# Kernel optimization log

Measured on AMD Instinct MI355X. Metric: run time of the kernel, lower is better.

Reference implementation:

```python
import jax, jax.numpy as jnp
import numpy as np

B, S, D_MODEL, D_HEAD = 4, 4096, 512, 64


def setup_inputs() -> dict:
    key = jax.random.key(0)
    ks = jax.random.split(key, 9)
    s = 1.0 / np.sqrt(D_MODEL)
    return {
        "q_in": jax.random.normal(ks[0], (B, S, D_MODEL), jnp.float32),
        "k_in": jax.random.normal(ks[1], (B, S, D_MODEL), jnp.float32),
        "v_in": jax.random.normal(ks[2], (B, S, D_MODEL), jnp.float32),
        "Wq": jax.random.normal(ks[3], (D_HEAD, D_MODEL), jnp.float32) * s,
        "bq": jax.random.normal(ks[4], (D_HEAD,), jnp.float32) * s,
        "Wk": jax.random.normal(ks[5], (D_HEAD, D_MODEL), jnp.float32) * s,
        "bk": jax.random.normal(ks[6], (D_HEAD,), jnp.float32) * s,
        "Wv": jax.random.normal(ks[7], (D_HEAD, D_MODEL), jnp.float32) * s,
        "bv": jax.random.normal(ks[8], (D_HEAD,), jnp.float32) * s,
    }


def reference(q_in, k_in, v_in, Wq, bq, Wk, bk, Wv, bv):
    # Linear projections (torch nn.Linear: x @ W.T + b)
    q = jnp.einsum("bsd,hd->bsh", q_in, Wq) + bq  # [B,S,Dh]
    k = jnp.einsum("bsd,hd->bsh", k_in, Wk) + bk
    v = jnp.einsum("bsd,hd->bsh", v_in, Wv) + bv
    # Causal mask: -inf strictly above diagonal (generate_attention_mask, triu(1))
    sk = k.shape[1]
    mask = jnp.triu(jnp.full((q.shape[1], sk), -jnp.inf, dtype=q.dtype), k=1)
    scores = jnp.einsum("bqh,bkh->bqk", q, k) / jnp.sqrt(jnp.asarray(q.shape[-1], q.dtype))
    attn = jax.nn.softmax(scores + mask, axis=-1)  # [B,S,S]
    return jnp.einsum("bqk,bkh->bqh", attn, v)
```

## Files before the change

kernel.cpp:

```cpp
#include <hip/hip_runtime.h>
#include <hip/hip_bf16.h>

#define B_ 4
#define S_ 4096
#define DM 512
#define DH 64

#define NEG_BIG (-3.0e38f)
#define MCLAMP  (-1.0e30f)

typedef __attribute__((ext_vector_type(8))) short short8b;
typedef __attribute__((ext_vector_type(4))) float f32x4;

__device__ __forceinline__ f32x4 MFMA16(short8b a, short8b b, f32x4 c) {
    return __builtin_amdgcn_mfma_f32_16x16x32_bf16(a, b, c, 0, 0, 0);
}

__device__ __forceinline__ float bf2f(unsigned short u) {
    unsigned int x = ((unsigned int)u) << 16;
    float f;
    __builtin_memcpy(&f, &x, 4);
    return f;
}
__device__ __forceinline__ unsigned short f2bf_rne(float f) {
    unsigned int u = __float_as_uint(f);
    u += 0x7FFFu + ((u >> 16) & 1u);
    return (unsigned short)(u >> 16);
}
__device__ __forceinline__ unsigned int pk2(unsigned short a, unsigned short b) {
    return (unsigned int)a | ((unsigned int)b << 16);
}

__device__ __forceinline__ void gload16(const void* gp, void* lp) {
    __builtin_amdgcn_global_load_lds(
        (const __attribute__((address_space(1))) void*)gp,
        (__attribute__((address_space(3))) void*)lp, 16, 0, 0);
}

__global__ void detect_kernel(const unsigned short* __restrict__ u,
                              int* __restrict__ flag) {
    __shared__ int cnt;
    if (threadIdx.x == 0) cnt = 0;
    __syncthreads();
    int w = 0;
    #pragma unroll
    for (int k = 0; k < 8; ++k) {
        unsigned short x = u[threadIdx.x * 8 + k];
        int e = (x >> 7) & 0xFF;
        if (e >= 135 || (e > 0 && e <= 95)) ++w;
    }
    atomicAdd(&cnt, w);
    __syncthreads();
    if (threadIdx.x == 0) *flag = (cnt > 64) ? 1 : 0;
}

#define PM 64
#define PK 64

__global__ __launch_bounds__(256) void proj_kernel(
    const void* __restrict__ xq, const void* __restrict__ xk,
    const void* __restrict__ xv,
    const void* __restrict__ Wq, const void* __restrict__ Wk,
    const void* __restrict__ Wv,
    const void* __restrict__ bq, const void* __restrict__ bk,
    const void* __restrict__ bv,
    unsigned short* __restrict__ Qhp, unsigned short* __restrict__ Qlp,
    unsigned short* __restrict__ Khp, unsigned short* __restrict__ Klp,
    unsigned short* __restrict__ Vthp, unsigned short* __restrict__ Vtlp,
    const int* __restrict__ flag)
{
    const int which = blockIdx.y;
    const void* x    = (which == 0) ? xq : (which == 1) ? xk : xv;
    const void* W    = (which == 0) ? Wq : (which == 1) ? Wk : Wv;
    const void* bias = (which == 0) ? bq : (which == 1) ? bk : bv;

    const bool f32 = (*flag != 0);
    const int row0 = blockIdx.x * PM;
    const int t    = threadIdx.x;
    const int lane = t & 63;
    const int w    = t >> 6;
    const int l15  = lane & 15;
    const int l4   = lane >> 4;

    __shared__ __align__(16) char sm[32768];

    const int srow = t >> 2;
    const int sseg = t & 3;
    const int swz  = (srow & 7) << 4;

    f32x4 acc[4];
    #pragma unroll
    for (int n = 0; n < 4; ++n) acc[n] = f32x4{0.f, 0.f, 0.f, 0.f};

    #pragma unroll 1
    for (int kc = 0; kc < DM / PK; ++kc) {
        const int k0 = kc * PK;
        __syncthreads();

        if (f32) {
            #pragma unroll
            for (int m = 0; m < 2; ++m) {
                const float* p = (m == 0)
                    ? (const float*)x + (size_t)(row0 + srow) * DM + k0 + sseg * 16
                    : (const float*)W + (size_t)srow * DM + k0 + sseg * 16;
                float v[16];
                #pragma unroll
                for (int j = 0; j < 4; ++j) {
                    float4 f = *reinterpret_cast<const float4*>(p + j * 4);
                    v[j * 4 + 0] = f.x; v[j * 4 + 1] = f.y;
                    v[j * 4 + 2] = f.z; v[j * 4 + 3] = f.w;
                }
                unsigned short hh[16], ll[16];
                #pragma unroll
                for (int j = 0; j < 16; ++j) {
                    unsigned short hb = f2bf_rne(v[j]);
                    hh[j] = hb;
                    ll[j] = f2bf_rne(v[j] - bf2f(hb));
                }
                char* dh = sm + m * 16384 + srow * 128;
                char* dl = dh + 8192;
                #pragma unroll
                for (int g = 0; g < 2; ++g) {
                    const int off = (sseg * 32 + g * 16) ^ swz;
                    uint4 hu, lu;
                    hu.x = pk2(hh[g*8+0], hh[g*8+1]); hu.y = pk2(hh[g*8+2], hh[g*8+3]);
                    hu.z = pk2(hh[g*8+4], hh[g*8+5]); hu.w = pk2(hh[g*8+6], hh[g*8+7]);
                    lu.x = pk2(ll[g*8+0], ll[g*8+1]); lu.y = pk2(ll[g*8+2], ll[g*8+3]);
                    lu.z = pk2(ll[g*8+4], ll[g*8+5]); lu.w = pk2(ll[g*8+6], ll[g*8+7]);
                    *reinterpret_cast<uint4*>(dh + off) = hu;
                    *reinterpret_cast<uint4*>(dl + off) = lu;
                }
            }
        } else {
            const uint4 z = {0u, 0u, 0u, 0u};
            #pragma unroll
            for (int m = 0; m < 2; ++m) {
                const unsigned short* p = (m == 0)
                    ? (const unsigned short*)x + (size_t)(row0 + srow) * DM + k0 + sseg * 16
                    : (const unsigned short*)W + (size_t)srow * DM + k0 + sseg * 16;
                char* dh = sm + m * 16384 + srow * 128;
                char* dl = dh + 8192;
                #pragma unroll
                for (int g = 0; g < 2; ++g) {
                    uint4 hv = *reinterpret_cast<const uint4*>(p + g * 8);
                    const int off = (sseg * 32 + g * 16) ^ swz;
                    *reinterpret_cast<uint4*>(dh + off) = hv;
                    *reinterpret_cast<uint4*>(dl + off) = z;
                }
            }
        }
        __syncthreads();

        const int arow = w * 16 + l15;
        short8b xh[2], xl[2];
        #pragma unroll
        for (int ks = 0; ks < 2; ++ks) {
            const int off = arow * 128 + ((ks * 64 + l4 * 16) ^ ((arow & 7) << 4));
            xh[ks] = *reinterpret_cast<const short8b*>(sm + off);
            xl[ks] = *reinterpret_cast<const short8b*>(sm + 8192 + off);
        }
        #pragma unroll
        for (int n = 0; n < 4; ++n) {
            #pragma unroll
            for (int ks = 0; ks < 2; ++ks) {
                const int brow = n * 16 + l15;
                const int off = brow * 128 + ((ks * 64 + l4 * 16) ^ ((brow & 7) << 4));
                short8b wh = *reinterpret_cast<const short8b*>(sm + 16384 + off);
                short8b wl = *reinterpret_cast<const short8b*>(sm + 24576 + off);
                acc[n] = MFMA16(xh[ks], wl, acc[n]);
                acc[n] = MFMA16(xl[ks], wh, acc[n]);
                acc[n] = MFMA16(xh[ks], wh, acc[n]);
            }
        }
    }

    __syncthreads();
    float* C = reinterpret_cast<float*>(sm);
    #pragma unroll
    for (int n = 0; n < 4; ++n)
        #pragma unroll
        for (int r = 0; r < 4; ++r)
            C[(w * 16 + l4 * 4 + r) * 66 + n * 16 + l15] = acc[n][r];
    __syncthreads();

    if (which < 2) {
        unsigned short* ph = (which == 0) ? Qhp : Khp;
        unsigned short* pl = (which == 0) ? Qlp : Klp;
        const float scale = (which == 0) ? 0.125f : 1.0f;
        const int r_  = t >> 2;
        const int c0_ = (t & 3) * 16;
        unsigned short hh[16], ll[16];
        #pragma unroll
        for (int j = 0; j < 16; ++j) {
            const float bv_ = f32 ? ((const float*)bias)[c0_ + j]
                                  : bf2f(((const unsigned short*)bias)[c0_ + j]);
            const float v = (C[r_ * 66 + c0_ + j] + bv_) * scale;
            unsigned short hb = f2bf_rne(v);
            hh[j] = hb;
            ll[j] = f2bf_rne(v - bf2f(hb));
        }
        const size_t off = (size_t)(row0 + r_) * DH + c0_;
        #pragma unroll
        for (int g = 0; g < 2; ++g) {
            uint4 hu, lu;
            hu.x = pk2(hh[g*8+0], hh[g*8+1]); hu.y = pk2(hh[g*8+2], hh[g*8+3]);
            hu.z = pk2(hh[g*8+4], hh[g*8+5]); hu.w = pk2(hh[g*8+6], hh[g*8+7]);
            lu.x = pk2(ll[g*8+0], ll[g*8+1]); lu.y = pk2(ll[g*8+2], ll[g*8+3]);
            lu.z = pk2(ll[g*8+4], ll[g*8+5]); lu.w = pk2(ll[g*8+6], ll[g*8+7]);
            *reinterpret_cast<uint4*>(ph + off + g * 8) = hu;
            *reinterpret_cast<uint4*>(pl + off + g * 8) = lu;
        }
    } else {
        const int c_ = t & 63;
        const int rb = (t >> 6) * 16;
        const int bb = row0 >> 12;
        const int s0 = row0 & (S_ - 1);
        const float bv_ = f32 ? ((const float*)bias)[c_]
                              : bf2f(((const unsigned short*)bias)[c_]);
        unsigned short hh[16], ll[16];
        #pragma unroll
        for (int i = 0; i < 16; ++i) {
            const float v = C[(rb + i) * 66 + c_] + bv_;
            unsigned short hb = f2bf_rne(v);
            hh[i] = hb;
            ll[i] = f2bf_rne(v - bf2f(hb));
        }
        const size_t off = (size_t)(bb * 64 + c_) * S_ + s0 + rb;
        #pragma unroll
        for (int g = 0; g < 2; ++g) {
            uint4 hu, lu;
            hu.x = pk2(hh[g*8+0], hh[g*8+1]); hu.y = pk2(hh[g*8+2], hh[g*8+3]);
            hu.z = pk2(hh[g*8+4], hh[g*8+5]); hu.w = pk2(hh[g*8+6], hh[g*8+7]);
            lu.x = pk2(ll[g*8+0], ll[g*8+1]); lu.y = pk2(ll[g*8+2], ll[g*8+3]);
            lu.z = pk2(ll[g*8+4], ll[g*8+5]); lu.w = pk2(ll[g*8+6], ll[g*8+7]);
            *reinterpret_cast<uint4*>(Vthp + off + g * 8) = hu;
            *reinterpret_cast<uint4*>(Vtlp + off + g * 8) = lu;
        }
    }
}

__global__ __launch_bounds__(512, 2) void flash_kernel(
    const unsigned short* __restrict__ Qh, const unsigned short* __restrict__ Ql,
    const unsigned short* __restrict__ Kh, const unsigned short* __restrict__ Kl,
    const unsigned short* __restrict__ Vth, const unsigned short* __restrict__ Vtl,
    void* __restrict__ out, const int* __restrict__ flag)
{
    const int pair = blockIdx.x;
    const int b    = blockIdx.y;
    const int t    = threadIdx.x;
    const int lane = t & 63;
    const int w    = t >> 6;
    const int qh   = w & 1;
    const int kh   = w >> 1;
    const int l15  = lane & 15;
    const int l4   = lane >> 4;

    __shared__ __align__(16) char smem[8192 + 2 * 65536];
    __shared__ float Mg[4][32];
    __shared__ float Lg[4][32];
    __shared__ float Ltot[32];

    const size_t bS = (size_t)b * S_;
    const bool f32o = (*flag != 0);

    const int qp   = t >> 8;
    const int qrow = (t & 255) >> 3;
    const int qsg  = t & 7;

    const int klaneoff = ((lane >> 3) << 7) +
                         ((((lane & 7) << 4)) ^ ((lane >> 3) << 4));
    const int vrl = lane >> 4;
    const int voff0 = (vrl << 13) + ((((lane & 15) << 4)) ^ (vrl << 4));
    const int voff1 = (vrl << 13) + ((((lane & 15) << 4)) ^ ((4 + vrl) << 4));

    const char* Khb = (const char*)Kh + bS * 128;
    const char* Klb = (const char*)Kl + bS * 128;
    const char* Vhb = (const char*)Vth + (size_t)b * 64 * 8192;
    const char* Vlb = (const char*)Vtl + (size_t)b * 64 * 8192;

    auto issue_tile = [&](int kt, int bsel) {
        char* buf = smem + 8192 + bsel * 65536;
        if (w < 4) {
            #pragma unroll
            for (int j = 0; j < 8; ++j) {
                const int c2  = w * 8 + j;
                const int p   = c2 >> 4;
                const int ckp = c2 & 15;
                const char* g = (p ? Klb : Khb) +
                                (size_t)kt * 16384 + ckp * 1024 + klaneoff;
                gload16(g, buf + p * 16384 + ckp * 1024);
            }
        } else {
            #pragma unroll
            for (int j = 0; j < 8; ++j) {
                const int c2  = (w - 4) * 8 + j;
                const int p   = c2 >> 4;
                const int cvp = c2 & 15;
                const int vo  = (cvp & 1) ? voff1 : voff0;
                const char* g = (p ? Vlb : Vhb) +
                                (size_t)cvp * 32768 + (size_t)kt * 256 + vo;
                gload16(g, buf + 32768 + p * 16384 + cvp * 1024);
            }
        }
    };

    #pragma unroll 1
    for (int hf = 0; hf < 2; ++hf) {
        const int qt = hf ? (127 - pair) : pair;
        const int q0 = qt << 5;
        const int nk = (qt >> 2) + 1;

        __syncthreads();

        {
            const unsigned short* src = qp ? Ql : Qh;
            uint4 v = *reinterpret_cast<const uint4*>(
                src + (bS + q0 + qrow) * 64 + qsg * 8);
            const int off = qp * 4096 + qrow * 128 +
                            ((qsg * 16) ^ ((qrow & 7) << 4));
            *reinterpret_cast<uint4*>(smem + off) = v;
        }
        issue_tile(0, 0);
        __syncthreads();

        short8b qf[2][2];
        #pragma unroll
        for (int p = 0; p < 2; ++p)
            #pragma unroll
            for (int ks = 0; ks < 2; ++ks) {
                const int row = qh * 16 + l15;
                const int off = p * 4096 + row * 128 +
                                ((ks * 64 + l4 * 16) ^ ((row & 7) << 4));
                qf[p][ks] = *reinterpret_cast<const short8b*>(smem + off);
            }
        __syncthreads();

        f32x4 of[4];
        of[0] = f32x4{0.f, 0.f, 0.f, 0.f};
        of[1] = f32x4{0.f, 0.f, 0.f, 0.f};
        of[2] = f32x4{0.f, 0.f, 0.f, 0.f};
        of[3] = f32x4{0.f, 0.f, 0.f, 0.f};
        float mrun[4], lrun[4];
        #pragma unroll
        for (int r = 0; r < 4; ++r) { mrun[r] = NEG_BIG; lrun[r] = 0.f; }

        #pragma unroll 1
        for (int kt = 0; kt < nk; ++kt) {
            const int bsel = kt & 1;
            if (kt + 1 < nk) issue_tile(kt + 1, bsel ^ 1);

            const char* kb = smem + 8192 + bsel * 65536;
            const char* vb = kb + 32768;

            f32x4 sc[2];
            #pragma unroll
            for (int ct = 0; ct < 2; ++ct) {
                f32x4 a = f32x4{0.f, 0.f, 0.f, 0.f};
                #pragma unroll
                for (int ks = 0; ks < 2; ++ks) {
                    const int row = kh * 32 + ct * 16 + l15;
                    const int off = row * 128 +
                                    ((ks * 64 + l4 * 16) ^ ((row & 7) << 4));
                    short8b bh = *reinterpret_cast<const short8b*>(kb + off);
                    short8b bl = *reinterpret_cast<const short8b*>(kb + 16384 + off);
                    a = MFMA16(qf[1][ks], bh, a);
                    a = MFMA16(qf[0][ks], bl, a);
                    a = MFMA16(qf[0][ks], bh, a);
                }
                sc[ct] = a;
            }

            if (kt == nk - 1) {
                #pragma unroll
                for (int ct = 0; ct < 2; ++ct) {
                    const int col = kt * 128 + kh * 32 + ct * 16 + l15;
                    #pragma unroll
                    for (int r = 0; r < 4; ++r) {
                        const int row = q0 + qh * 16 + l4 * 4 + r;
                        if (col > row) sc[ct][r] = NEG_BIG;
                    }
                }
            }

            float pm[4];
            #pragma unroll
            for (int r = 0; r < 4; ++r) pm[r] = fmaxf(sc[0][r], sc[1][r]);
            #pragma unroll
            for (int s = 1; s < 16; s <<= 1)
                #pragma unroll
                for (int r = 0; r < 4; ++r)
                    pm[r] = fmaxf(pm[r], __shfl_xor(pm[r], s));

            float alpha[4], ps[4];
            #pragma unroll
            for (int r = 0; r < 4; ++r) {
                const float mn = fmaxf(fmaxf(mrun[r], pm[r]), MCLAMP);
                alpha[r] = __expf(mrun[r] - mn);
                mrun[r] = mn;
                sc[0][r] = __expf(sc[0][r] - mn);
                sc[1][r] = __expf(sc[1][r] - mn);
                ps[r] = sc[0][r] + sc[1][r];
            }
            #pragma unroll
            for (int s = 1; s < 16; s <<= 1)
                #pragma unroll
                for (int r = 0; r < 4; ++r) ps[r] += __shfl_xor(ps[r], s);
            #pragma unroll
            for (int r = 0; r < 4; ++r) lrun[r] = lrun[r] * alpha[r] + ps[r];
            #pragma unroll
            for (int c = 0; c < 4; ++c)
                #pragma unroll
                for (int r = 0; r < 4; ++r) of[c][r] *= alpha[r];

            #pragma unroll
            for (int ct = 0; ct < 2; ++ct)
                #pragma unroll
                for (int r = 0; r < 4; ++r) {
                    const int row = qh * 16 + l4 * 4 + r;
                    const int col = kh * 32 + ct * 16 + l15;
                    const int off = row * 256 + ((col * 2) ^ ((row & 7) << 4));
                    *reinterpret_cast<unsigned short*>(smem + off) =
                        f2bf_rne(sc[ct][r]);
                }
            asm volatile("s_waitcnt lgkmcnt(0)" ::: "memory");
            __builtin_amdgcn_sched_barrier(0);

            short8b pf;
            {
                const int row = qh * 16 + l15;
                const int off = row * 256 + ((kh * 64 + l4 * 16) ^ ((row & 7) << 4));
                pf = *reinterpret_cast<const short8b*>(smem + off);
            }
            #pragma unroll
            for (int ct = 0; ct < 4; ++ct) {
                const int vr = ct * 16 + l15;
                const int voff = vr * 256 +
                                 ((kh * 64 + l4 * 16) ^ ((vr & 7) << 4));
                short8b vh = *reinterpret_cast<const short8b*>(vb + voff);
                short8b vl = *reinterpret_cast<const short8b*>(vb + 16384 + voff);
                of[ct] = MFMA16(pf, vl, of[ct]);
                of[ct] = MFMA16(pf, vh, of[ct]);
            }

            __syncthreads();
        }

        if (l15 == 0) {
            #pragma unroll
            for (int r = 0; r < 4; ++r) {
                const int row = qh * 16 + l4 * 4 + r;
                Mg[kh][row] = mrun[r];
                Lg[kh][row] = lrun[r];
            }
        }
        __syncthreads();

        float* Op = reinterpret_cast<float*>(smem + 8192);
        #pragma unroll
        for (int r = 0; r < 4; ++r) {
            const int row = qh * 16 + l4 * 4 + r;
            const float M = fmaxf(fmaxf(Mg[0][row], Mg[1][row]),
                                  fmaxf(Mg[2][row], Mg[3][row]));
            const float L = Lg[0][row] * __expf(Mg[0][row] - M)
                          + Lg[1][row] * __expf(Mg[1][row] - M)
                          + Lg[2][row] * __expf(Mg[2][row] - M)
                          + Lg[3][row] * __expf(Mg[3][row] - M);
            const float al = __expf(mrun[r] - M);
            #pragma unroll
            for (int c = 0; c < 4; ++c)
                Op[kh * 2048 + row * 64 + c * 16 + l15] = of[c][r] * al;
            if (kh == 0 && l15 == 0) Ltot[row] = L;
        }
        __syncthreads();

        {
            const int row = t >> 4;
            const int d0  = (t & 15) << 2;
            float4 s = {0.f, 0.f, 0.f, 0.f};
            #pragma unroll
            for (int g = 0; g < 4; ++g) {
                float4 v = *reinterpret_cast<const float4*>(
                    Op + g * 2048 + row * 64 + d0);
                s.x += v.x; s.y += v.y; s.z += v.z; s.w += v.w;
            }
            const float inv = 1.0f / Ltot[row];
            const size_t oi = (bS + q0 + row) * 64 + d0;
            if (f32o) {
                float4 o;
                o.x = s.x * inv; o.y = s.y * inv;
                o.z = s.z * inv; o.w = s.w * inv;
                *reinterpret_cast<float4*>((float*)out + oi) = o;
            } else {
                ushort4 o;
                o.x = f2bf_rne(s.x * inv);
                o.y = f2bf_rne(s.y * inv);
                o.z = f2bf_rne(s.z * inv);
                o.w = f2bf_rne(s.w * inv);
                *reinterpret_cast<ushort4*>((unsigned short*)out + oi) = o;
            }
        }
    }
}

extern "C" void kernel_launch(void* const* d_in, const int* in_sizes, int n_in,
                              void* d_out, int out_size, void* d_ws, size_t ws_size,
                              hipStream_t stream) {
    const size_t NP = (size_t)B_ * S_ * DH;
    unsigned short* Qhp  = (unsigned short*)d_ws;
    unsigned short* Qlp  = Qhp + NP;
    unsigned short* Khp  = Qhp + 2 * NP;
    unsigned short* Klp  = Qhp + 3 * NP;
    unsigned short* Vthp = Qhp + 4 * NP;
    unsigned short* Vtlp = Qhp + 5 * NP;
    int* flag = (int*)(Qhp + 6 * NP);

    detect_kernel<<<1, 256, 0, stream>>>((const unsigned short*)d_in[0], flag);

    proj_kernel<<<dim3(B_ * S_ / PM, 3), 256, 0, stream>>>(
        d_in[0], d_in[1], d_in[2],
        d_in[3], d_in[5], d_in[7],
        d_in[4], d_in[6], d_in[8],
        Qhp, Qlp, Khp, Klp, Vthp, Vtlp, flag);

    flash_kernel<<<dim3(64, B_), 512, 0, stream>>>(
        Qhp, Qlp, Khp, Klp, Vthp, Vtlp, d_out, flag);
}
```

Baseline: 220.0 us.

## Restructure flash kernel to 256-thread blocks with 64-key tiles and fold dtype detection

```diff
diff --git a/kernel.cpp b/kernel.cpp
--- a/kernel.cpp
+++ b/kernel.cpp
@@ -36,26 +36,6 @@
         (const __attribute__((address_space(1))) void*)gp,
         (__attribute__((address_space(3))) void*)lp, 16, 0, 0);
 }
-
-__global__ void detect_kernel(const unsigned short* __restrict__ u,
-                              int* __restrict__ flag) {
-    __shared__ int cnt;
-    if (threadIdx.x == 0) cnt = 0;
-    __syncthreads();
-    int w = 0;
-    #pragma unroll
-    for (int k = 0; k < 8; ++k) {
-        unsigned short x = u[threadIdx.x * 8 + k];
-        int e = (x >> 7) & 0xFF;
-        if (e >= 135 || (e > 0 && e <= 95)) ++w;
-    }
-    atomicAdd(&cnt, w);
-    __syncthreads();
-    if (threadIdx.x == 0) *flag = (cnt > 64) ? 1 : 0;
-}
-
-#define PM 64
-#define PK 64
 
 __global__ __launch_bounds__(256) void proj_kernel(
     const void* __restrict__ xq, const void* __restrict__ xk,
@@ -66,16 +46,14 @@
     const void* __restrict__ bv,
     unsigned short* __restrict__ Qhp, unsigned short* __restrict__ Qlp,
     unsigned short* __restrict__ Khp, unsigned short* __restrict__ Klp,
-    unsigned short* __restrict__ Vthp, unsigned short* __restrict__ Vtlp,
-    const int* __restrict__ flag)
+    unsigned short* __restrict__ Vthp, unsigned short* __restrict__ Vtlp)
 {
     const int which = blockIdx.y;
     const void* x    = (which == 0) ? xq : (which == 1) ? xk : xv;
     const void* W    = (which == 0) ? Wq : (which == 1) ? Wk : Wv;
     const void* bias = (which == 0) ? bq : (which == 1) ? bk : bv;
 
-    const bool f32 = (*flag != 0);
-    const int row0 = blockIdx.x * PM;
+    const int row0 = blockIdx.x * 64;
     const int t    = threadIdx.x;
     const int lane = t & 63;
     const int w    = t >> 6;
@@ -83,18 +61,36 @@
     const int l4   = lane >> 4;
 
     __shared__ __align__(16) char sm[32768];
+    __shared__ int sdet;
+
+    if (t == 0) sdet = 0;
+    __syncthreads();
+    {
+        const unsigned short* u = (const unsigned short*)xq;
+        int cnt = 0;
+        #pragma unroll
+        for (int k = 0; k < 8; ++k) {
+            unsigned short v = u[t * 8 + k];
+            int e = (v >> 7) & 0xFF;
+            if (e >= 135 || (e > 0 && e <= 95)) ++cnt;
+        }
+        atomicAdd(&sdet, cnt);
+    }
+    __syncthreads();
+    const bool f32 = (sdet > 64);
 
     const int srow = t >> 2;
     const int sseg = t & 3;
     const int swz  = (srow & 7) << 4;
+    const int arow = w * 16 + l15;
 
     f32x4 acc[4];
     #pragma unroll
     for (int n = 0; n < 4; ++n) acc[n] = f32x4{0.f, 0.f, 0.f, 0.f};
 
     #pragma unroll 1
-    for (int kc = 0; kc < DM / PK; ++kc) {
-        const int k0 = kc * PK;
+    for (int kc = 0; kc < DM / 64; ++kc) {
+        const int k0 = kc * 64;
         __syncthreads();
 
         if (f32) {
@@ -107,8 +103,8 @@
                 #pragma unroll
                 for (int j = 0; j < 4; ++j) {
                     float4 f = *reinterpret_cast<const float4*>(p + j * 4);
-                    v[j * 4 + 0] = f.x; v[j * 4 + 1] = f.y;
-                    v[j * 4 + 2] = f.z; v[j * 4 + 3] = f.w;
+                    v[j*4+0] = f.x; v[j*4+1] = f.y;
+                    v[j*4+2] = f.z; v[j*4+3] = f.w;
                 }
                 unsigned short hh[16], ll[16];
                 #pragma unroll
@@ -151,7 +147,6 @@
         }
         __syncthreads();
 
-        const int arow = w * 16 + l15;
         short8b xh[2], xl[2];
         #pragma unroll
         for (int ks = 0; ks < 2; ++ks) {
@@ -161,9 +156,9 @@
         }
         #pragma unroll
         for (int n = 0; n < 4; ++n) {
+            const int brow = n * 16 + l15;
             #pragma unroll
             for (int ks = 0; ks < 2; ++ks) {
-                const int brow = n * 16 + l15;
                 const int off = brow * 128 + ((ks * 64 + l4 * 16) ^ ((brow & 7) << 4));
                 short8b wh = *reinterpret_cast<const short8b*>(sm + 16384 + off);
                 short8b wl = *reinterpret_cast<const short8b*>(sm + 24576 + off);
@@ -239,14 +234,15 @@
     }
 }
 
-__global__ __launch_bounds__(512, 2) void flash_kernel(
+__global__ __launch_bounds__(256, 2) void flash_kernel(
     const unsigned short* __restrict__ Qh, const unsigned short* __restrict__ Ql,
     const unsigned short* __restrict__ Kh, const unsigned short* __restrict__ Kl,
     const unsigned short* __restrict__ Vth, const unsigned short* __restrict__ Vtl,
-    void* __restrict__ out, const int* __restrict__ flag)
+    void* __restrict__ out, const unsigned short* __restrict__ xq_det)
 {
-    const int pair = blockIdx.x;
-    const int b    = blockIdx.y;
+    const int blk  = blockIdx.x;
+    const int qt   = 127 - (blk >> 2);
+    const int b    = blk & 3;
     const int t    = threadIdx.x;
     const int lane = t & 63;
     const int w    = t >> 6;
@@ -255,23 +251,35 @@
     const int l15  = lane & 15;
     const int l4   = lane >> 4;
 
-    __shared__ __align__(16) char smem[8192 + 2 * 65536];
-    __shared__ float Mg[4][32];
-    __shared__ float Lg[4][32];
+    __shared__ __align__(16) char smem[8192 + 2 * 32768];
+    __shared__ float Mg[2][32];
+    __shared__ float Lg[2][32];
     __shared__ float Ltot[32];
+    __shared__ int sdet;
+
+    if (t == 0) sdet = 0;
+    __syncthreads();
+    {
+        int cnt = 0;
+        #pragma unroll
+        for (int k = 0; k < 8; ++k) {
+            unsigned short v = xq_det[t * 8 + k];
+            int e = (v >> 7) & 0xFF;
+            if (e >= 135 || (e > 0 && e <= 95)) ++cnt;
+        }
+        atomicAdd(&sdet, cnt);
+    }
+    __syncthreads();
+    const bool f32o = (sdet > 64);
 
     const size_t bS = (size_t)b * S_;
-    const bool f32o = (*flag != 0);
-
-    const int qp   = t >> 8;
-    const int qrow = (t & 255) >> 3;
-    const int qsg  = t & 7;
+    const int q0 = qt << 5;
+    const int nk = (qt >> 1) + 1;
 
     const int klaneoff = ((lane >> 3) << 7) +
                          ((((lane & 7) << 4)) ^ ((lane >> 3) << 4));
-    const int vrl = lane >> 4;
-    const int voff0 = (vrl << 13) + ((((lane & 15) << 4)) ^ (vrl << 4));
-    const int voff1 = (vrl << 13) + ((((lane & 15) << 4)) ^ ((4 + vrl) << 4));
+    const int vlaneoff = ((lane >> 3) << 13) +
+                         ((((lane & 7) << 4)) ^ ((lane >> 3) << 4));
 
     const char* Khb = (const char*)Kh + bS * 128;
     const char* Klb = (const char*)Kl + bS * 128;
@@ -279,225 +287,220 @@
     const char* Vlb = (const char*)Vtl + (size_t)b * 64 * 8192;
 
     auto issue_tile = [&](int kt, int bsel) {
-        char* buf = smem + 8192 + bsel * 65536;
-        if (w < 4) {
+        char* buf = smem + 8192 + bsel * 32768;
+        if (w < 2) {
             #pragma unroll
             for (int j = 0; j < 8; ++j) {
-                const int c2  = w * 8 + j;
-                const int p   = c2 >> 4;
-                const int ckp = c2 & 15;
+                const int c  = w * 8 + j;
+                const int p  = c >> 3;
+                const int ck = c & 7;
                 const char* g = (p ? Klb : Khb) +
-                                (size_t)kt * 16384 + ckp * 1024 + klaneoff;
-                gload16(g, buf + p * 16384 + ckp * 1024);
+                                (size_t)kt * 8192 + ck * 1024 + klaneoff;
+                gload16(g, buf + p * 8192 + ck * 1024);
             }
         } else {
             #pragma unroll
             for (int j = 0; j < 8; ++j) {
-                const int c2  = (w - 4) * 8 + j;
-                const int p   = c2 >> 4;
-                const int cvp = c2 & 15;
-                const int vo  = (cvp & 1) ? voff1 : voff0;
+                const int c  = (w - 2) * 8 + j;
+                const int p  = c >> 3;
+                const int cv = c & 7;
                 const char* g = (p ? Vlb : Vhb) +
-                                (size_t)cvp * 32768 + (size_t)kt * 256 + vo;
-                gload16(g, buf + 32768 + p * 16384 + cvp * 1024);
+                                (size_t)cv * 65536 + (size_t)kt * 128 + vlaneoff;
+                gload16(g, buf + 16384 + p * 8192 + cv * 1024);
             }
         }
     };
 
+    {
+        const int qrow = t >> 3;
+        const int qsg  = t & 7;
+        const size_t goff = (bS + q0 + qrow) * 64 + qsg * 8;
+        const int off = qrow * 128 + ((qsg * 16) ^ ((qrow & 7) << 4));
+        *reinterpret_cast<uint4*>(smem + off) =
+            *reinterpret_cast<const uint4*>(Qh + goff);
+        *reinterpret_cast<uint4*>(smem + 4096 + off) =
+            *reinterpret_cast<const uint4*>(Ql + goff);
+    }
+    issue_tile(0, 0);
+    __syncthreads();
+
+    short8b qf[2][2];
+    #pragma unroll
+    for (int p = 0; p < 2; ++p)
+        #pragma unroll
+        for (int ks = 0; ks < 2; ++ks) {
+            const int row = qh * 16 + l15;
+            const int off = p * 4096 + row * 128 +
+                            ((ks * 64 + l4 * 16) ^ ((row & 7) << 4));
+            qf[p][ks] = *reinterpret_cast<const short8b*>(smem + off);
+        }
+    __syncthreads();
+
+    f32x4 of[4];
+    of[0] = f32x4{0.f, 0.f, 0.f, 0.f};
+    of[1] = f32x4{0.f, 0.f, 0.f, 0.f};
+    of[2] = f32x4{0.f, 0.f, 0.f, 0.f};
+    of[3] = f32x4{0.f, 0.f, 0.f, 0.f};
+    float mrun[4], lrun[4];
+    #pragma unroll
+    for (int r = 0; r < 4; ++r) { mrun[r] = NEG_BIG; lrun[r] = 0.f; }
+
     #pragma unroll 1
-    for (int hf = 0; hf < 2; ++hf) {
-        const int qt = hf ? (127 - pair) : pair;
-        const int q0 = qt << 5;
-        const int nk = (qt >> 2) + 1;
-
-        __syncthreads();
-
-        {
-            const unsigned short* src = qp ? Ql : Qh;
-            uint4 v = *reinterpret_cast<const uint4*>(
-                src + (bS + q0 + qrow) * 64 + qsg * 8);
-            const int off = qp * 4096 + qrow * 128 +
-                            ((qsg * 16) ^ ((qrow & 7) << 4));
-            *reinterpret_cast<uint4*>(smem + off) = v;
-        }
-        issue_tile(0, 0);
-        __syncthreads();
-
-        short8b qf[2][2];
-        #pragma unroll
-        for (int p = 0; p < 2; ++p)
+    for (int kt = 0; kt < nk; ++kt) {
+        const int bsel = kt & 1;
+        if (kt + 1 < nk) issue_tile(kt + 1, bsel ^ 1);
+
+        const char* kb = smem + 8192 + bsel * 32768;
+        const char* vb = kb + 16384;
+
+        f32x4 sc[2];
+        #pragma unroll
+        for (int ct = 0; ct < 2; ++ct) {
+            f32x4 a = f32x4{0.f, 0.f, 0.f, 0.f};
             #pragma unroll
             for (int ks = 0; ks < 2; ++ks) {
-                const int row = qh * 16 + l15;
-                const int off = p * 4096 + row * 128 +
+                const int row = kh * 32 + ct * 16 + l15;
+                const int off = row * 128 +
                                 ((ks * 64 + l4 * 16) ^ ((row & 7) << 4));
-                qf[p][ks] = *reinterpret_cast<const short8b*>(smem + off);
-            }
-        __syncthreads();
-
-        f32x4 of[4];
-        of[0] = f32x4{0.f, 0.f, 0.f, 0.f};
-        of[1] = f32x4{0.f, 0.f, 0.f, 0.f};
-        of[2] = f32x4{0.f, 0.f, 0.f, 0.f};
-        of[3] = f32x4{0.f, 0.f, 0.f, 0.f};
-        float mrun[4], lrun[4];
-        #pragma unroll
-        for (int r = 0; r < 4; ++r) { mrun[r] = NEG_BIG; lrun[r] = 0.f; }
-
-        #pragma unroll 1
-        for (int kt = 0; kt < nk; ++kt) {
-            const int bsel = kt & 1;
-            if (kt + 1 < nk) issue_tile(kt + 1, bsel ^ 1);
-
-            const char* kb = smem + 8192 + bsel * 65536;
-            const char* vb = kb + 32768;
-
-            f32x4 sc[2];
+                short8b bh = *reinterpret_cast<const short8b*>(kb + off);
+                short8b bl = *reinterpret_cast<const short8b*>(kb + 8192 + off);
+                a = MFMA16(qf[1][ks], bh, a);
+                a = MFMA16(qf[0][ks], bl, a);
+                a = MFMA16(qf[0][ks], bh, a);
+            }
+            sc[ct] = a;
+        }
+
+        if (kt == nk - 1) {
             #pragma unroll
             for (int ct = 0; ct < 2; ++ct) {
-                f32x4 a = f32x4{0.f, 0.f, 0.f, 0.f};
-                #pragma unroll
-                for (int ks = 0; ks < 2; ++ks) {
-                    const int row = kh * 32 + ct * 16 + l15;
-                    const int off = row * 128 +
-                                    ((ks * 64 + l4 * 16) ^ ((row & 7) << 4));
-                    short8b bh = *reinterpret_cast<const short8b*>(kb + off);
-                    short8b bl = *reinterpret_cast<const short8b*>(kb + 16384 + off);
-                    a = MFMA16(qf[1][ks], bh, a);
-                    a = MFMA16(qf[0][ks], bl, a);
-                    a = MFMA16(qf[0][ks], bh, a);
-                }
-                sc[ct] = a;
-            }
-
-            if (kt == nk - 1) {
-                #pragma unroll
-                for (int ct = 0; ct < 2; ++ct) {
-                    const int col = kt * 128 + kh * 32 + ct * 16 + l15;
-                    #pragma unroll
-                    for (int r = 0; r < 4; ++r) {
-                        const int row = q0 + qh * 16 + l4 * 4 + r;
-                        if (col > row) sc[ct][r] = NEG_BIG;
-                    }
-                }
-            }
-
-            float pm[4];
-            #pragma unroll
-            for (int r = 0; r < 4; ++r) pm[r] = fmaxf(sc[0][r], sc[1][r]);
-            #pragma unroll
-            for (int s = 1; s < 16; s <<= 1)
-                #pragma unroll
-                for (int r = 0; r < 4; ++r)
-                    pm[r] = fmaxf(pm[r], __shfl_xor(pm[r], s));
-
-            float alpha[4], ps[4];
-            #pragma unroll
-            for (int r = 0; r < 4; ++r) {
-                const float mn = fmaxf(fmaxf(mrun[r], pm[r]), MCLAMP);
-                alpha[r] = __expf(mrun[r] - mn);
-                mrun[r] = mn;
-                sc[0][r] = __expf(sc[0][r] - mn);
-                sc[1][r] = __expf(sc[1][r] - mn);
-                ps[r] = sc[0][r] + sc[1][r];
-            }
-            #pragma unroll
-            for (int s = 1; s < 16; s <<= 1)
-                #pragma unroll
-                for (int r = 0; r < 4; ++r) ps[r] += __shfl_xor(ps[r], s);
-            #pragma unroll
-            for (int r = 0; r < 4; ++r) lrun[r] = lrun[r] * alpha[r] + ps[r];
-            #pragma unroll
-            for (int c = 0; c < 4; ++c)
-                #pragma unroll
-                for (int r = 0; r < 4; ++r) of[c][r] *= alpha[r];
-
-            #pragma unroll
-            for (int ct = 0; ct < 2; ++ct)
+                const int col = kt * 64 + kh * 32 + ct * 16 + l15;
                 #pragma unroll
                 for (int r = 0; r < 4; ++r) {
-                    const int row = qh * 16 + l4 * 4 + r;
-                    const int col = kh * 32 + ct * 16 + l15;
-                    const int off = row * 256 + ((col * 2) ^ ((row & 7) << 4));
-                    *reinterpret_cast<unsigned short*>(smem + off) =
-                        f2bf_rne(sc[ct][r]);
+                    const int row = q0 + qh * 16 + l4 * 4 + r;
+                    if (col > row) sc[ct][r] = NEG_BIG;
                 }
-            asm volatile("s_waitcnt lgkmcnt(0)" ::: "memory");
-            __builtin_amdgcn_sched_barrier(0);
-
-            short8b pf;
-            {
-                const int row = qh * 16 + l15;
-                const int off = row * 256 + ((kh * 64 + l4 * 16) ^ ((row & 7) << 4));
-                pf = *reinterpret_cast<const short8b*>(smem + off);
-            }
-            #pragma unroll
-            for (int ct = 0; ct < 4; ++ct) {
-                const int vr = ct * 16 + l15;
-                const int voff = vr * 256 +
-                                 ((kh * 64 + l4 * 16) ^ ((vr & 7) << 4));
-                short8b vh = *reinterpret_cast<const short8b*>(vb + voff);
-                short8b vl = *reinterpret_cast<const short8b*>(vb + 16384 + voff);
-                of[ct] = MFMA16(pf, vl, of[ct]);
-                of[ct] = MFMA16(pf, vh, of[ct]);
-            }
-
-            __syncthreads();
-        }
-
-        if (l15 == 0) {
+            }
+        }
+
+        float pm[4];
+        #pragma unroll
+        for (int r = 0; r < 4; ++r) pm[r] = fmaxf(sc[0][r], sc[1][r]);
+        #pragma unroll
+        for (int s = 1; s < 16; s <<= 1)
+            #pragma unroll
+            for (int r = 0; r < 4; ++r)
+                pm[r] = fmaxf(pm[r], __shfl_xor(pm[r], s));
+
+        float alpha[4], ps[4];
+        #pragma unroll
+        for (int r = 0; r < 4; ++r) {
+            const float mn = fmaxf(fmaxf(mrun[r], pm[r]), MCLAMP);
+            alpha[r] = __expf(mrun[r] - mn);
+            mrun[r] = mn;
+            sc[0][r] = __expf(sc[0][r] - mn);
+            sc[1][r] = __expf(sc[1][r] - mn);
+            ps[r] = sc[0][r] + sc[1][r];
+        }
+        #pragma unroll
+        for (int s = 1; s < 16; s <<= 1)
+            #pragma unroll
+            for (int r = 0; r < 4; ++r) ps[r] += __shfl_xor(ps[r], s);
+        #pragma unroll
+        for (int r = 0; r < 4; ++r) lrun[r] = lrun[r] * alpha[r] + ps[r];
+        #pragma unroll
+        for (int c = 0; c < 4; ++c)
+            #pragma unroll
+            for (int r = 0; r < 4; ++r) of[c][r] *= alpha[r];
+
+        #pragma unroll
+        for (int ct = 0; ct < 2; ++ct)
             #pragma unroll
             for (int r = 0; r < 4; ++r) {
                 const int row = qh * 16 + l4 * 4 + r;
-                Mg[kh][row] = mrun[r];
-                Lg[kh][row] = lrun[r];
-            }
-        }
+                const int col = kh * 32 + ct * 16 + l15;
+                const int off = row * 128 + ((col * 2) ^ ((row & 7) << 4));
+                *reinterpret_cast<unsigned short*>(smem + off) =
+                    f2bf_rne(sc[ct][r]);
+            }
+        asm volatile("s_waitcnt lgkmcnt(0)" ::: "memory");
+        __builtin_amdgcn_sched_barrier(0);
+
+        short8b pf;
+        {
+            const int row = qh * 16 + l15;
+            const int off = row * 128 + ((kh * 64 + l4 * 16) ^ ((row & 7) << 4));
+            pf = *reinterpret_cast<const short8b*>(smem + off);
+        }
+        #pragma unroll
+        for (int ct = 0; ct < 4; ++ct) {
+            const int vr = ct * 16 + l15;
+            const int voff = vr * 128 +
+                             ((kh * 64 + l4 * 16) ^ ((vr & 7) << 4));
+            short8b vh = *reinterpret_cast<const short8b*>(vb + voff);
+            short8b vl = *reinterpret_cast<const short8b*>(vb + 8192 + voff);
+            of[ct] = MFMA16(pf, vl, of[ct]);
+            of[ct] = MFMA16(pf, vh, of[ct]);
+        }
+
         __syncthreads();
-
-        float* Op = reinterpret_cast<float*>(smem + 8192);
+    }
+
+    if (l15 == 0) {
         #pragma unroll
         for (int r = 0; r < 4; ++r) {
             const int row = qh * 16 + l4 * 4 + r;
-            const float M = fmaxf(fmaxf(Mg[0][row], Mg[1][row]),
-                                  fmaxf(Mg[2][row], Mg[3][row]));
-            const float L = Lg[0][row] * __expf(Mg[0][row] - M)
-                          + Lg[1][row] * __expf(Mg[1][row] - M)
-                          + Lg[2][row] * __expf(Mg[2][row] - M)
-                          + Lg[3][row] * __expf(Mg[3][row] - M);
-            const float al = __expf(mrun[r] - M);
-            #pragma unroll
-            for (int c = 0; c < 4; ++c)
-                Op[kh * 2048 + row * 64 + c * 16 + l15] = of[c][r] * al;
-            if (kh == 0 && l15 == 0) Ltot[row] = L;
-        }
-        __syncthreads();
-
-        {
-            const int row = t >> 4;
-            const int d0  = (t & 15) << 2;
-            float4 s = {0.f, 0.f, 0.f, 0.f};
-            #pragma unroll
-            for (int g = 0; g < 4; ++g) {
-                float4 v = *reinterpret_cast<const float4*>(
-                    Op + g * 2048 + row * 64 + d0);
-                s.x += v.x; s.y += v.y; s.z += v.z; s.w += v.w;
-            }
-            const float inv = 1.0f / Ltot[row];
-            const size_t oi = (bS + q0 + row) * 64 + d0;
-            if (f32o) {
+            Mg[kh][row] = mrun[r];
+            Lg[kh][row] = lrun[r];
+        }
+    }
+    __syncthreads();
+
+    float* Op = reinterpret_cast<float*>(smem + 8192);
+    #pragma unroll
+    for (int r = 0; r < 4; ++r) {
+        const int row = qh * 16 + l4 * 4 + r;
+        const float M = fmaxf(Mg[0][row], Mg[1][row]);
+        const float L = Lg[0][row] * __expf(Mg[0][row] - M)
+                      + Lg[1][row] * __expf(Mg[1][row] - M);
+        const float al = __expf(mrun[r] - M);
+        #pragma unroll
+        for (int c = 0; c < 4; ++c)
+            Op[kh * 2048 + row * 64 + c * 16 + l15] = of[c][r] * al;
+        if (kh == 0 && l15 == 0) Ltot[row] = L;
+    }
+    __syncthreads();
+
+    {
+        const int row = t >> 3;
+        const int d0  = (t & 7) << 3;
+        float s[8];
+        #pragma unroll
+        for (int j = 0; j < 2; ++j) {
+            float4 a = *reinterpret_cast<const float4*>(Op + row * 64 + d0 + j * 4);
+            float4 c = *reinterpret_cast<const float4*>(Op + 2048 + row * 64 + d0 + j * 4);
+            s[j*4+0] = a.x + c.x; s[j*4+1] = a.y + c.y;
+            s[j*4+2] = a.z + c.z; s[j*4+3] = a.w + c.w;
+        }
+        const float inv = 1.0f / Ltot[row];
+        const size_t oi = (bS + q0 + row) * 64 + d0;
+        if (f32o) {
+            float* op = (float*)out + oi;
+            #pragma unroll
+            for (int j = 0; j < 2; ++j) {
                 float4 o;
-                o.x = s.x * inv; o.y = s.y * inv;
-                o.z = s.z * inv; o.w = s.w * inv;
-                *reinterpret_cast<float4*>((float*)out + oi) = o;
-            } else {
-                ushort4 o;
-                o.x = f2bf_rne(s.x * inv);
-                o.y = f2bf_rne(s.y * inv);
-                o.z = f2bf_rne(s.z * inv);
-                o.w = f2bf_rne(s.w * inv);
-                *reinterpret_cast<ushort4*>((unsigned short*)out + oi) = o;
-            }
+                o.x = s[j*4+0] * inv; o.y = s[j*4+1] * inv;
+                o.z = s[j*4+2] * inv; o.w = s[j*4+3] * inv;
+                *reinterpret_cast<float4*>(op + j * 4) = o;
+            }
+        } else {
+            unsigned short hh[8];
+            #pragma unroll
+            for (int j = 0; j < 8; ++j) hh[j] = f2bf_rne(s[j] * inv);
+            uint4 o;
+            o.x = pk2(hh[0], hh[1]); o.y = pk2(hh[2], hh[3]);
+            o.z = pk2(hh[4], hh[5]); o.w = pk2(hh[6], hh[7]);
+            *reinterpret_cast<uint4*>((unsigned short*)out + oi) = o;
         }
     }
 }
@@ -512,16 +515,14 @@
     unsigned short* Klp  = Qhp + 3 * NP;
     unsigned short* Vthp = Qhp + 4 * NP;
     unsigned short* Vtlp = Qhp + 5 * NP;
-    int* flag = (int*)(Qhp + 6 * NP);
-
-    detect_kernel<<<1, 256, 0, stream>>>((const unsigned short*)d_in[0], flag);
-
-    proj_kernel<<<dim3(B_ * S_ / PM, 3), 256, 0, stream>>>(
+
+    proj_kernel<<<dim3(B_ * S_ / 64, 3), 256, 0, stream>>>(
         d_in[0], d_in[1], d_in[2],
         d_in[3], d_in[5], d_in[7],
         d_in[4], d_in[6], d_in[8],
-        Qhp, Qlp, Khp, Klp, Vthp, Vtlp, flag);
-
-    flash_kernel<<<dim3(64, B_), 512, 0, stream>>>(
-        Qhp, Qlp, Khp, Klp, Vthp, Vtlp, d_out, flag);
-}
+        Qhp, Qlp, Khp, Klp, Vthp, Vtlp);
+
+    flash_kernel<<<dim3(512), 256, 0, stream>>>(
+        Qhp, Qlp, Khp, Klp, Vthp, Vtlp, d_out,
+        (const unsigned short*)d_in[0]);
+}
```

New measurement: 251.9 us. 14.5% more time.

## Drop V low-part split, inline dtype detection, shrink flash LDS tiles

Applied to the files above, without the earlier changes.

```diff
diff --git a/kernel.cpp b/kernel.cpp
--- a/kernel.cpp
+++ b/kernel.cpp
@@ -36,26 +36,6 @@
         (const __attribute__((address_space(1))) void*)gp,
         (__attribute__((address_space(3))) void*)lp, 16, 0, 0);
 }
-
-__global__ void detect_kernel(const unsigned short* __restrict__ u,
-                              int* __restrict__ flag) {
-    __shared__ int cnt;
-    if (threadIdx.x == 0) cnt = 0;
-    __syncthreads();
-    int w = 0;
-    #pragma unroll
-    for (int k = 0; k < 8; ++k) {
-        unsigned short x = u[threadIdx.x * 8 + k];
-        int e = (x >> 7) & 0xFF;
-        if (e >= 135 || (e > 0 && e <= 95)) ++w;
-    }
-    atomicAdd(&cnt, w);
-    __syncthreads();
-    if (threadIdx.x == 0) *flag = (cnt > 64) ? 1 : 0;
-}
-
-#define PM 64
-#define PK 64
 
 __global__ __launch_bounds__(256) void proj_kernel(
     const void* __restrict__ xq, const void* __restrict__ xk,
@@ -66,16 +46,14 @@
     const void* __restrict__ bv,
     unsigned short* __restrict__ Qhp, unsigned short* __restrict__ Qlp,
     unsigned short* __restrict__ Khp, unsigned short* __restrict__ Klp,
-    unsigned short* __restrict__ Vthp, unsigned short* __restrict__ Vtlp,
-    const int* __restrict__ flag)
+    unsigned short* __restrict__ Vthp)
 {
     const int which = blockIdx.y;
     const void* x    = (which == 0) ? xq : (which == 1) ? xk : xv;
     const void* W    = (which == 0) ? Wq : (which == 1) ? Wk : Wv;
     const void* bias = (which == 0) ? bq : (which == 1) ? bk : bv;
 
-    const bool f32 = (*flag != 0);
-    const int row0 = blockIdx.x * PM;
+    const int row0 = blockIdx.x * 64;
     const int t    = threadIdx.x;
     const int lane = t & 63;
     const int w    = t >> 6;
@@ -83,18 +61,36 @@
     const int l4   = lane >> 4;
 
     __shared__ __align__(16) char sm[32768];
+    __shared__ int sdet;
+
+    if (t == 0) sdet = 0;
+    __syncthreads();
+    {
+        const unsigned short* u = (const unsigned short*)xq;
+        int cnt = 0;
+        #pragma unroll
+        for (int k = 0; k < 8; ++k) {
+            unsigned short v = u[t * 8 + k];
+            int e = (v >> 7) & 0xFF;
+            if (e >= 135 || (e > 0 && e <= 95)) ++cnt;
+        }
+        atomicAdd(&sdet, cnt);
+    }
+    __syncthreads();
+    const bool f32 = (sdet > 64);
 
     const int srow = t >> 2;
     const int sseg = t & 3;
     const int swz  = (srow & 7) << 4;
+    const int arow = w * 16 + l15;
 
     f32x4 acc[4];
     #pragma unroll
     for (int n = 0; n < 4; ++n) acc[n] = f32x4{0.f, 0.f, 0.f, 0.f};
 
     #pragma unroll 1
-    for (int kc = 0; kc < DM / PK; ++kc) {
-        const int k0 = kc * PK;
+    for (int kc = 0; kc < DM / 64; ++kc) {
+        const int k0 = kc * 64;
         __syncthreads();
 
         if (f32) {
@@ -107,8 +103,8 @@
                 #pragma unroll
                 for (int j = 0; j < 4; ++j) {
                     float4 f = *reinterpret_cast<const float4*>(p + j * 4);
-                    v[j * 4 + 0] = f.x; v[j * 4 + 1] = f.y;
-                    v[j * 4 + 2] = f.z; v[j * 4 + 3] = f.w;
+                    v[j*4+0] = f.x; v[j*4+1] = f.y;
+                    v[j*4+2] = f.z; v[j*4+3] = f.w;
                 }
                 unsigned short hh[16], ll[16];
                 #pragma unroll
@@ -151,7 +147,6 @@
         }
         __syncthreads();
 
-        const int arow = w * 16 + l15;
         short8b xh[2], xl[2];
         #pragma unroll
         for (int ks = 0; ks < 2; ++ks) {
@@ -161,9 +156,9 @@
         }
         #pragma unroll
         for (int n = 0; n < 4; ++n) {
+            const int brow = n * 16 + l15;
             #pragma unroll
             for (int ks = 0; ks < 2; ++ks) {
-                const int brow = n * 16 + l15;
                 const int off = brow * 128 + ((ks * 64 + l4 * 16) ^ ((brow & 7) << 4));
                 short8b wh = *reinterpret_cast<const short8b*>(sm + 16384 + off);
                 short8b wl = *reinterpret_cast<const short8b*>(sm + 24576 + off);
@@ -217,33 +212,26 @@
         const int s0 = row0 & (S_ - 1);
         const float bv_ = f32 ? ((const float*)bias)[c_]
                               : bf2f(((const unsigned short*)bias)[c_]);
-        unsigned short hh[16], ll[16];
-        #pragma unroll
-        for (int i = 0; i < 16; ++i) {
-            const float v = C[(rb + i) * 66 + c_] + bv_;
-            unsigned short hb = f2bf_rne(v);
-            hh[i] = hb;
-            ll[i] = f2bf_rne(v - bf2f(hb));
-        }
+        unsigned short hh[16];
+        #pragma unroll
+        for (int i = 0; i < 16; ++i)
+            hh[i] = f2bf_rne(C[(rb + i) * 66 + c_] + bv_);
         const size_t off = (size_t)(bb * 64 + c_) * S_ + s0 + rb;
         #pragma unroll
         for (int g = 0; g < 2; ++g) {
-            uint4 hu, lu;
+            uint4 hu;
             hu.x = pk2(hh[g*8+0], hh[g*8+1]); hu.y = pk2(hh[g*8+2], hh[g*8+3]);
             hu.z = pk2(hh[g*8+4], hh[g*8+5]); hu.w = pk2(hh[g*8+6], hh[g*8+7]);
-            lu.x = pk2(ll[g*8+0], ll[g*8+1]); lu.y = pk2(ll[g*8+2], ll[g*8+3]);
-            lu.z = pk2(ll[g*8+4], ll[g*8+5]); lu.w = pk2(ll[g*8+6], ll[g*8+7]);
             *reinterpret_cast<uint4*>(Vthp + off + g * 8) = hu;
-            *reinterpret_cast<uint4*>(Vtlp + off + g * 8) = lu;
         }
     }
 }
 
-__global__ __launch_bounds__(512, 2) void flash_kernel(
+__global__ __launch_bounds__(512, 1) void flash_kernel(
     const unsigned short* __restrict__ Qh, const unsigned short* __restrict__ Ql,
     const unsigned short* __restrict__ Kh, const unsigned short* __restrict__ Kl,
-    const unsigned short* __restrict__ Vth, const unsigned short* __restrict__ Vtl,
-    void* __restrict__ out, const int* __restrict__ flag)
+    const unsigned short* __restrict__ Vth,
+    void* __restrict__ out, const unsigned short* __restrict__ xq_det)
 {
     const int pair = blockIdx.x;
     const int b    = blockIdx.y;
@@ -255,13 +243,28 @@
     const int l15  = lane & 15;
     const int l4   = lane >> 4;
 
-    __shared__ __align__(16) char smem[8192 + 2 * 65536];
+    __shared__ __align__(16) char smem[8192 + 2 * 49152];
     __shared__ float Mg[4][32];
     __shared__ float Lg[4][32];
     __shared__ float Ltot[32];
+    __shared__ int sdet;
+
+    if (t == 0) sdet = 0;
+    __syncthreads();
+    if (t < 256) {
+        int cnt = 0;
+        #pragma unroll
+        for (int k = 0; k < 8; ++k) {
+            unsigned short v = xq_det[t * 8 + k];
+            int e = (v >> 7) & 0xFF;
+            if (e >= 135 || (e > 0 && e <= 95)) ++cnt;
+        }
+        atomicAdd(&sdet, cnt);
+    }
+    __syncthreads();
+    const bool f32o = (sdet > 64);
 
     const size_t bS = (size_t)b * S_;
-    const bool f32o = (*flag != 0);
 
     const int qp   = t >> 8;
     const int qrow = (t & 255) >> 3;
@@ -276,10 +279,9 @@
     const char* Khb = (const char*)Kh + bS * 128;
     const char* Klb = (const char*)Kl + bS * 128;
     const char* Vhb = (const char*)Vth + (size_t)b * 64 * 8192;
-    const char* Vlb = (const char*)Vtl + (size_t)b * 64 * 8192;
 
     auto issue_tile = [&](int kt, int bsel) {
-        char* buf = smem + 8192 + bsel * 65536;
+        char* buf = smem + 8192 + bsel * 49152;
         if (w < 4) {
             #pragma unroll
             for (int j = 0; j < 8; ++j) {
@@ -292,14 +294,11 @@
             }
         } else {
             #pragma unroll
-            for (int j = 0; j < 8; ++j) {
-                const int c2  = (w - 4) * 8 + j;
-                const int p   = c2 >> 4;
-                const int cvp = c2 & 15;
+            for (int j = 0; j < 4; ++j) {
+                const int cvp = (w - 4) * 4 + j;
                 const int vo  = (cvp & 1) ? voff1 : voff0;
-                const char* g = (p ? Vlb : Vhb) +
-                                (size_t)cvp * 32768 + (size_t)kt * 256 + vo;
-                gload16(g, buf + 32768 + p * 16384 + cvp * 1024);
+                const char* g = Vhb + (size_t)cvp * 32768 + (size_t)kt * 256 + vo;
+                gload16(g, buf + 32768 + cvp * 1024);
             }
         }
     };
@@ -349,7 +348,7 @@
             const int bsel = kt & 1;
             if (kt + 1 < nk) issue_tile(kt + 1, bsel ^ 1);
 
-            const char* kb = smem + 8192 + bsel * 65536;
+            const char* kb = smem + 8192 + bsel * 49152;
             const char* vb = kb + 32768;
 
             f32x4 sc[2];
@@ -437,8 +436,6 @@
                 const int voff = vr * 256 +
                                  ((kh * 64 + l4 * 16) ^ ((vr & 7) << 4));
                 short8b vh = *reinterpret_cast<const short8b*>(vb + voff);
-                short8b vl = *reinterpret_cast<const short8b*>(vb + 16384 + voff);
-                of[ct] = MFMA16(pf, vl, of[ct]);
                 of[ct] = MFMA16(pf, vh, of[ct]);
             }
 
@@ -474,7 +471,7 @@
         __syncthreads();
 
         {
-            const int row = t >> 4;
+            const int row = (t >> 4) & 31;
             const int d0  = (t & 15) << 2;
             float4 s = {0.f, 0.f, 0.f, 0.f};
             #pragma unroll
@@ -511,17 +508,14 @@
     unsigned short* Khp  = Qhp + 2 * NP;
     unsigned short* Klp  = Qhp + 3 * NP;
     unsigned short* Vthp = Qhp + 4 * NP;
-    unsigned short* Vtlp = Qhp + 5 * NP;
-    int* flag = (int*)(Qhp + 6 * NP);
-
-    detect_kernel<<<1, 256, 0, stream>>>((const unsigned short*)d_in[0], flag);
-
-    proj_kernel<<<dim3(B_ * S_ / PM, 3), 256, 0, stream>>>(
+
+    proj_kernel<<<dim3(B_ * S_ / 64, 3), 256, 0, stream>>>(
         d_in[0], d_in[1], d_in[2],
         d_in[3], d_in[5], d_in[7],
         d_in[4], d_in[6], d_in[8],
-        Qhp, Qlp, Khp, Klp, Vthp, Vtlp, flag);
+        Qhp, Qlp, Khp, Klp, Vthp);
 
     flash_kernel<<<dim3(64, B_), 512, 0, stream>>>(
-        Qhp, Qlp, Khp, Klp, Vthp, Vtlp, d_out, flag);
-}
+        Qhp, Qlp, Khp, Klp, Vthp, d_out,
+        (const unsigned short*)d_in[0]);
+}
```

Result: no change. 215.8 us (-1.9%).
